# Kernel tuning notes

Hardware: AMD Instinct MI355X
Metric: run time of the kernel (lower is better)

## Reference

```python
import jax, jax.numpy as jnp
import numpy as np

HEADS = 8
DIM_HEAD = 64
SLICE = 64
DIM = 128
INNER = HEADS * DIM_HEAD
B, H, W = 4, 128, 128


def _conv(x_nchw, w_oihw, b):
    y = jax.lax.conv_general_dilated(
        x_nchw, w_oihw, window_strides=(1, 1), padding='SAME',
        dimension_numbers=('NCHW', 'OIHW', 'NCHW'))
    return y + b[None, :, None, None]


def setup_inputs() -> dict:
    key = jax.random.key(0)
    ks = jax.random.split(key, 10)
    s = lambda fan: 1.0 / np.sqrt(fan)
    return {
        'x': jax.random.normal(ks[0], (B, H, W, DIM), jnp.float32),
        'temperature': jnp.ones((1, HEADS, 1, 1), jnp.float32) * 0.5,
        'Wx': jax.random.normal(ks[1], (INNER, DIM, 3, 3), jnp.float32) * s(DIM * 9),
        'bx': jnp.zeros((INNER,), jnp.float32),
        'Wfx': jax.random.normal(ks[2], (INNER, DIM, 3, 3), jnp.float32) * s(DIM * 9),
        'bfx': jnp.zeros((INNER,), jnp.float32),
        'Ws': jax.random.normal(ks[3], (SLICE, DIM_HEAD), jnp.float32) * s(DIM_HEAD),
        'bs': jnp.zeros((SLICE,), jnp.float32),
        'Wq': jax.random.normal(ks[4], (DIM_HEAD, DIM_HEAD), jnp.float32) * s(DIM_HEAD),
        'Wk': jax.random.normal(ks[5], (DIM_HEAD, DIM_HEAD), jnp.float32) * s(DIM_HEAD),
        'Wv': jax.random.normal(ks[6], (DIM_HEAD, DIM_HEAD), jnp.float32) * s(DIM_HEAD),
        'Wo': jax.random.normal(ks[7], (DIM, INNER), jnp.float32) * s(INNER),
        'bo': jnp.zeros((DIM,), jnp.float32),
    }


def reference(x, temperature, Wx, bx, Wfx, bfx, Ws, bs, Wq, Wk, Wv, Wo, bo):
    b, h, w, _ = x.shape
    n = h * w
    scale = DIM_HEAD ** -0.5
    x_nchw = jnp.transpose(x, (0, 3, 1, 2))
    # conv projections -> [B, heads, N, dim_head]
    def to_heads(y):
        y = jnp.transpose(y, (0, 2, 3, 1)).reshape(b, n, HEADS, DIM_HEAD)
        return jnp.transpose(y, (0, 2, 1, 3))
    fx_mid = to_heads(_conv(x_nchw, Wfx, bfx))
    x_mid = to_heads(_conv(x_nchw, Wx, bx))
    # slice routing: softmax over M, temperature-scaled
    temp = jnp.clip(temperature, 0.1, 5.0)  # [1,heads,1,1]
    logits = (jnp.einsum('bhnc,gc->bhng', x_mid, Ws) + bs) / temp
    slice_weights = jax.nn.softmax(logits, axis=-1)  # [B,h,N,M]
    slice_norm = slice_weights.sum(axis=2)  # [B,h,M]
    slice_token = jnp.einsum('bhnc,bhng->bhgc', fx_mid, slice_weights)
    slice_token = slice_token / (slice_norm + 1e-5)[..., None]
    # small M x M attention over slice tokens
    q = jnp.einsum('bhgc,dc->bhgd', slice_token, Wq)
    k = jnp.einsum('bhgc,dc->bhgd', slice_token, Wk)
    v = jnp.einsum('bhgc,dc->bhgd', slice_token, Wv)
    dots = jnp.einsum('bhgd,bhkd->bhgk', q, k) * scale
    attn = jax.nn.softmax(dots, axis=-1)
    out_slice = jnp.einsum('bhgk,bhkd->bhgd', attn, v)
    # scatter back to points
    out_x = jnp.einsum('bhgc,bhng->bhnc', out_slice, slice_weights)
    out_x = jnp.transpose(out_x, (0, 2, 1, 3)).reshape(b, h, w, INNER)
    return jnp.einsum('bhwi,oi->bhwo', out_x, Wo) + bo
```

## Files before the change

### kernel.cpp

```cpp
#include <hip/hip_runtime.h>
#include <hip/hip_bf16.h>
#include <math.h>

#define B_ 4
#define H_ 128
#define W_ 128
#define DIM_ 128
#define HEADS_ 8
#define DH_ 64
#define G_ 64
#define INNER_ 512
#define N_ 16384

typedef __attribute__((ext_vector_type(8))) short sh8;
typedef __attribute__((ext_vector_type(4))) float vf4;

#define XPT_SLAB 4160
#define XPT_PLANE 2163200
#define WT_PLANE 1179648

__device__ __forceinline__ void gload16(const void* g, void* l) {
  __builtin_amdgcn_global_load_lds((const __attribute__((address_space(1))) void*)g,
                                   (__attribute__((address_space(3))) void*)l, 16, 0, 0);
}

__device__ __forceinline__ void split_bf16(float v, ushort& h, ushort& l) {
  __hip_bfloat16 hb = __float2bfloat16(v);
  float hf = __bfloat162float(hb);
  __hip_bfloat16 lb = __float2bfloat16(v - hf);
  h = *reinterpret_cast<ushort*>(&hb);
  l = *reinterpret_cast<ushort*>(&lb);
}

__global__ __launch_bounds__(256) void pad_tile_kernel(const float* __restrict__ x,
                                                       ushort* __restrict__ xpth,
                                                       ushort* __restrict__ xptl) {
  const int bz = blockIdx.y;
  x += (size_t)bz * N_ * DIM_;
  xpth += (size_t)bz * XPT_PLANE;
  xptl += (size_t)bz * XPT_PLANE;
  const int idx = blockIdx.x * 256 + threadIdx.x;
  const int row = idx / (4 * XPT_SLAB);
  const int rem = idx % (4 * XPT_SLAB);
  const int c0i = rem / XPT_SLAB;
  const int t2 = rem % XPT_SLAB;
  const int tile = t2 >> 3, j = t2 & 7;
  const int kg = tile / 130, px = tile % 130;
  const int c = c0i * 32 + kg * 8 + j;
  float v = 0.0f;
  if (row >= 1 && row <= H_ && px >= 1 && px <= W_)
    v = x[((size_t)(row - 1) * W_ + (px - 1)) * DIM_ + c];
  ushort hh, ll;
  split_bf16(v, hh, ll);
  xpth[idx] = hh;
  xptl[idx] = ll;
}

__global__ __launch_bounds__(256) void wfx_kernel(const float* __restrict__ Wfx,
                                                  ushort* __restrict__ wth,
                                                  ushort* __restrict__ wtl) {
  int idx = blockIdx.x * 256 + threadIdx.x;
  if (idx >= 9 * 512 * DIM_) return;
  const int c = idx & 127;
  const int ocf = (idx >> 7) & 511;
  const int tap = idx >> 16;
  float v = Wfx[((size_t)ocf * DIM_ + c) * 9 + tap];
  ushort hh, ll;
  split_bf16(v, hh, ll);
  const int nt = 4 + (ocf >> 7), oci = ocf & 127;
  const int c0i = c >> 5, kg = (c >> 3) & 3, j = c & 7;
  const size_t o = (((size_t)tap * 8 + nt) * 4 + c0i) * 4096 + ((size_t)kg * 128 + oci) * 8 + j;
  wth[o] = hh;
  wtl[o] = ll;
}

__global__ __launch_bounds__(256) void wcomp_kernel(const float* __restrict__ Wx,
                                                    const float* __restrict__ Ws,
                                                    const float* __restrict__ bx,
                                                    const float* __restrict__ bs,
                                                    const float* __restrict__ temperature,
                                                    ushort* __restrict__ wth,
                                                    ushort* __restrict__ wtl,
                                                    float* __restrict__ bc) {
  __shared__ float WxL[64][128];
  __shared__ float WsL[64][64];
  const int t = threadIdx.x;
  const int tap = blockIdx.x, h = blockIdx.y;
  for (int e = t; e < 8192; e += 256) {
    const int c2 = e >> 7, c = e & 127;
    WxL[c2][c] = Wx[((size_t)(h * 64 + c2) * DIM_ + c) * 9 + tap];
  }
  for (int e = t; e < 4096; e += 256) WsL[e >> 6][e & 63] = Ws[e];
  float tmp = fminf(fmaxf(temperature[h], 0.1f), 5.0f);
  const float invt = 1.0f / tmp;
  __syncthreads();
  for (int e = t; e < 8192; e += 256) {
    const int gg = e >> 7, c = e & 127;
    float s = 0.f;
#pragma unroll
    for (int c2 = 0; c2 < 64; ++c2) s = fmaf(WsL[gg][c2], WxL[c2][c], s);
    s *= invt;
    ushort hh, ll;
    split_bf16(s, hh, ll);
    const int ocp = h * 64 + gg;
    const int nt = ocp >> 7, oci = ocp & 127;
    const int c0i = c >> 5, kg = (c >> 3) & 3, j = c & 7;
    const size_t o = (((size_t)tap * 8 + nt) * 4 + c0i) * 4096 + ((size_t)kg * 128 + oci) * 8 + j;
    wth[o] = hh;
    wtl[o] = ll;
  }
  if (tap == 0 && t < 64) {
    float s = 0.f;
#pragma unroll
    for (int c2 = 0; c2 < 64; ++c2) s = fmaf(Ws[t * 64 + c2], bx[h * 64 + c2], s);
    bc[h * 64 + t] = (s + bs[t]) * invt;
  }
}

__global__ __launch_bounds__(256) void mqk_kernel(const float* __restrict__ Wq,
                                                  const float* __restrict__ Wk,
                                                  float* __restrict__ mqk) {
  const int idx = blockIdx.x * 256 + threadIdx.x;
  const int c = idx >> 6, c2 = idx & 63;
  float s = 0.f;
#pragma unroll
  for (int d = 0; d < 64; ++d) s = fmaf(Wq[d * 64 + c], Wk[d * 64 + c2], s);
  mqk[idx] = s * 0.125f;
}

__global__ __launch_bounds__(256) void conv_mfma_kernel(
    const ushort* __restrict__ xpth, const ushort* __restrict__ xptl,
    const ushort* __restrict__ wth, const ushort* __restrict__ wtl,
    const float* __restrict__ bc, const float* __restrict__ bfx,
    float* __restrict__ lg, float* __restrict__ fxo) {
  __shared__ __align__(16) ushort lds[16512];
  const int bz = blockIdx.z;
  xpth += (size_t)bz * XPT_PLANE;
  xptl += (size_t)bz * XPT_PLANE;
  lg += (size_t)bz * N_ * INNER_;
  fxo += (size_t)bz * N_ * INNER_;
  const int t = threadIdx.x;
  const int lane = t & 63;
  const int wid = t >> 6;
  const int wm = wid & 1, wn = wid >> 1;
  const int nt = blockIdx.x;
  const int y = blockIdx.y;
  const int col = lane & 15, quad = lane >> 4;

  vf4 acc[4][4];
#pragma unroll
  for (int i = 0; i < 4; ++i)
#pragma unroll
    for (int j = 0; j < 4; ++j) acc[i][j] = vf4{0.f, 0.f, 0.f, 0.f};

  auto stageB = [&](int tap, int c0i) {
    const size_t boff = (((size_t)tap * 8 + nt) * 4 + c0i) * 4096;
    gload16(wth + boff + t * 8, lds + 8320 + t * 8);
    gload16(wth + boff + 2048 + t * 8, lds + 8320 + 2048 + t * 8);
    gload16(wtl + boff + t * 8, lds + 12416 + t * 8);
    gload16(wtl + boff + 2048 + t * 8, lds + 12416 + 2048 + t * 8);
  };

  for (int ky = 0; ky < 3; ++ky) {
    for (int c0i = 0; c0i < 4; ++c0i) {
      const size_t aoff = ((size_t)(y + ky) * 4 + c0i) * XPT_SLAB;
      __syncthreads();
      gload16(xpth + aoff + t * 8, lds + t * 8);
      gload16(xpth + aoff + 2048 + t * 8, lds + 2048 + t * 8);
      gload16(xptl + aoff + t * 8, lds + 4160 + t * 8);
      gload16(xptl + aoff + 2048 + t * 8, lds + 4160 + 2048 + t * 8);
      if (t < 8) {
        *reinterpret_cast<sh8*>(lds + 4096 + t * 8) =
            *reinterpret_cast<const sh8*>(xpth + aoff + 4096 + t * 8);
        *reinterpret_cast<sh8*>(lds + 4160 + 4096 + t * 8) =
            *reinterpret_cast<const sh8*>(xptl + aoff + 4096 + t * 8);
      }
      stageB(ky * 3, c0i);
      __syncthreads();
      for (int kx = 0; kx < 3; ++kx) {
        sh8 ah[4], al[4], bh[4], bl[4];
#pragma unroll
        for (int j = 0; j < 4; ++j) {
          const int brd = (quad * 128 + wn * 64 + j * 16 + col) * 8;
          bh[j] = *reinterpret_cast<const sh8*>(lds + 8320 + brd);
          bl[j] = *reinterpret_cast<const sh8*>(lds + 12416 + brd);
        }
#pragma unroll
        for (int i = 0; i < 4; ++i) {
          const int ard = (quad * 130 + wm * 64 + i * 16 + col + kx) * 8;
          ah[i] = *reinterpret_cast<const sh8*>(lds + ard);
          al[i] = *reinterpret_cast<const sh8*>(lds + 4160 + ard);
        }
        if (kx < 2) {
          __syncthreads();
          stageB(ky * 3 + kx + 1, c0i);
        }
        __builtin_amdgcn_s_setprio(1);
#pragma unroll
        for (int i = 0; i < 4; ++i)
#pragma unroll
          for (int j = 0; j < 4; ++j) {
            acc[i][j] = __builtin_amdgcn_mfma_f32_16x16x32_bf16(ah[i], bh[j], acc[i][j], 0, 0, 0);
            acc[i][j] = __builtin_amdgcn_mfma_f32_16x16x32_bf16(ah[i], bl[j], acc[i][j], 0, 0, 0);
            acc[i][j] = __builtin_amdgcn_mfma_f32_16x16x32_bf16(al[i], bh[j], acc[i][j], 0, 0, 0);
          }
        __builtin_amdgcn_s_setprio(0);
        if (kx < 2) __syncthreads();
      }
    }
  }
  const bool first = (nt < 4);
  float* outp = first ? lg : fxo;
  const float* bb = first ? bc : bfx;
  const int ocbase = (nt & 3) * 128 + wn * 64 + col;
#pragma unroll
  for (int j = 0; j < 4; ++j) {
    const int oc = ocbase + j * 16;
    const float bv = bb[oc];
#pragma unroll
    for (int i = 0; i < 4; ++i) {
#pragma unroll
      for (int r = 0; r < 4; ++r) {
        const int px = wm * 64 + i * 16 + quad * 4 + r;
        outp[((size_t)(y * W_ + px)) * INNER_ + oc] = acc[i][j][r] + bv;
      }
    }
  }
}

__device__ __forceinline__ void fma16(float (&acc)[4][4], const float4 a, const float4 b) {
  acc[0][0] = fmaf(a.x, b.x, acc[0][0]);
  acc[0][1] = fmaf(a.x, b.y, acc[0][1]);
  acc[0][2] = fmaf(a.x, b.z, acc[0][2]);
  acc[0][3] = fmaf(a.x, b.w, acc[0][3]);
  acc[1][0] = fmaf(a.y, b.x, acc[1][0]);
  acc[1][1] = fmaf(a.y, b.y, acc[1][1]);
  acc[1][2] = fmaf(a.y, b.z, acc[1][2]);
  acc[1][3] = fmaf(a.y, b.w, acc[1][3]);
  acc[2][0] = fmaf(a.z, b.x, acc[2][0]);
  acc[2][1] = fmaf(a.z, b.y, acc[2][1]);
  acc[2][2] = fmaf(a.z, b.z, acc[2][2]);
  acc[2][3] = fmaf(a.z, b.w, acc[2][3]);
  acc[3][0] = fmaf(a.w, b.x, acc[3][0]);
  acc[3][1] = fmaf(a.w, b.y, acc[3][1]);
  acc[3][2] = fmaf(a.w, b.z, acc[3][2]);
  acc[3][3] = fmaf(a.w, b.w, acc[3][3]);
}

__global__ __launch_bounds__(256) void slice_kernel(float* __restrict__ lg,
                                                    const float* __restrict__ fxg,
                                                    float* __restrict__ tpart,
                                                    float* __restrict__ npart) {
  __shared__ __align__(16) float wl[64][68];
  __shared__ __align__(16) float fxl[64][68];
  __shared__ float red[8][64];
  const int bz = blockIdx.y;
  lg += (size_t)bz * N_ * INNER_;
  fxg += (size_t)bz * N_ * INNER_;
  tpart += (size_t)bz * 512 * 4096;
  npart += (size_t)bz * 512 * 64;
  unsigned int* lgp = reinterpret_cast<unsigned int*>(lg);

  const int t = threadIdx.x;
  const int sub = blockIdx.x & 63;
  const int h = blockIdx.x >> 6;
  const int nbase = sub * 256;
  const int tx = t & 15;
  const int ty = t >> 4;
  const int sn = t >> 2;
  const int sq = t & 3;
  const int gg2 = t & 63;
  const int q2 = t >> 6;

  float acc2[4][4] = {};
  float snrmp = 0.0f;

  for (int s = 0; s < 4; ++s) {
    const int n0 = nbase + s * 64;
    __syncthreads();
    {
      const int cg = t & 15;
      const int nr = t >> 4;
#pragma unroll
      for (int r = 0; r < 4; ++r) {
        const int nn = nr + r * 16;
        const size_t rowoff = ((size_t)(n0 + nn)) * INNER_ + h * DH_ + cg * 4;
        *reinterpret_cast<float4*>(&wl[nn][cg * 4]) =
            *reinterpret_cast<const float4*>(lg + rowoff);
        *reinterpret_cast<float4*>(&fxl[nn][cg * 4]) =
            *reinterpret_cast<const float4*>(fxg + rowoff);
      }
    }
    __syncthreads();
    float m = -3.4e38f;
#pragma unroll
    for (int jj = 0; jj < 16; ++jj) m = fmaxf(m, wl[sn][sq * 16 + jj]);
    red[sq][sn] = m;
    __syncthreads();
    m = fmaxf(fmaxf(red[0][sn], red[1][sn]), fmaxf(red[2][sn], red[3][sn]));
    float ss = 0.0f;
#pragma unroll
    for (int jj = 0; jj < 16; ++jj) {
      const float e = __expf(wl[sn][sq * 16 + jj] - m);
      wl[sn][sq * 16 + jj] = e;
      ss += e;
    }
    red[4 + sq][sn] = ss;
    __syncthreads();
    const float inv = 1.0f / (red[4][sn] + red[5][sn] + red[6][sn] + red[7][sn]);
#pragma unroll
    for (int jj = 0; jj < 16; ++jj) wl[sn][sq * 16 + jj] *= inv;
    __syncthreads();
    {
      const int gg = t & 15;
      const int nr = t >> 4;
#pragma unroll
      for (int r = 0; r < 4; ++r) {
        const int nn = nr + r * 16;
        uint4 pk;
        unsigned int* pp = reinterpret_cast<unsigned int*>(&pk);
#pragma unroll
        for (int j = 0; j < 4; ++j) {
          ushort hh, ll;
          split_bf16(wl[nn][gg * 4 + j], hh, ll);
          pp[j] = ((unsigned int)hh << 16) | (unsigned int)ll;
        }
        *reinterpret_cast<uint4*>(lgp + ((size_t)(n0 + nn)) * INNER_ + h * DH_ + gg * 4) = pk;
      }
    }
#pragma unroll
    for (int nn = 0; nn < 16; ++nn) snrmp += wl[q2 * 16 + nn][gg2];
#pragma unroll
    for (int kk = 0; kk < 64; ++kk) {
      const float4 a4 = *reinterpret_cast<const float4*>(&wl[kk][ty * 4]);
      const float4 b4 = *reinterpret_cast<const float4*>(&fxl[kk][tx * 4]);
      fma16(acc2, a4, b4);
    }
  }
  __syncthreads();
  red[q2][gg2] = snrmp;
  float* tp = tpart + (size_t)blockIdx.x * 4096;
#pragma unroll
  for (int i = 0; i < 4; ++i) {
    float4 v;
    v.x = acc2[i][0];
    v.y = acc2[i][1];
    v.z = acc2[i][2];
    v.w = acc2[i][3];
    *reinterpret_cast<float4*>(tp + (ty * 4 + i) * 64 + tx * 4) = v;
  }
  __syncthreads();
  if (t < 64)
    npart[(size_t)blockIdx.x * 64 + t] = red[0][t] + red[1][t] + red[2][t] + red[3][t];
}

__global__ __launch_bounds__(256) void reduce_kernel(const float* __restrict__ tpart,
                                                     const float* __restrict__ npart,
                                                     float* __restrict__ tok,
                                                     float* __restrict__ nrm) {
  const int bz = blockIdx.y;
  tpart += (size_t)bz * 512 * 4096;
  npart += (size_t)bz * 512 * 64;
  tok += (size_t)bz * (HEADS_ * G_ * DH_);
  nrm += (size_t)bz * (HEADS_ * G_);
  if (blockIdx.x < 128) {
    const int idx = blockIdx.x * 256 + threadIdx.x;
    const int h = idx >> 12, e = idx & 4095;
    float s = 0.f;
    for (int cb = 0; cb < 64; ++cb)
      s += tpart[(((size_t)(h * 64 + cb)) << 12) + e];
    tok[idx] = s;
  } else {
    for (int o = threadIdx.x; o < 512; o += 256) {
      const int h = o >> 6, g = o & 63;
      float s = 0.f;
      for (int cb = 0; cb < 64; ++cb) s += npart[(size_t)(h * 64 + cb) * 64 + g];
      nrm[o] = s;
    }
  }
}

__global__ __launch_bounds__(256) void head_kernel(const float* __restrict__ tok,
                                                   const float* __restrict__ nrm,
                                                   const float* __restrict__ mqk,
                                                   const float* __restrict__ Wv,
                                                   const float* __restrict__ Wo,
                                                   ushort* __restrict__ mht,
                                                   ushort* __restrict__ mlt) {
  __shared__ float ST[64 * 65];
  __shared__ float YL[64 * 64];
  __shared__ float VL[64 * 64];
  __shared__ float red[8][64];
  const int bz = blockIdx.y;
  tok += (size_t)bz * (HEADS_ * G_ * DH_);
  nrm += (size_t)bz * (HEADS_ * G_);
  mht += (size_t)bz * (INNER_ * DIM_);
  mlt += (size_t)bz * (INNER_ * DIM_);
  const int t = threadIdx.x;
  const int h = blockIdx.x;

  for (int e = t; e < 4096; e += 256) {
    const int g = e >> 6, c = e & 63;
    ST[g * 65 + c] = tok[(size_t)h * 4096 + e] / (nrm[h * 64 + g] + 1e-5f);
  }
  __syncthreads();
  for (int e = t; e < 4096; e += 256) {
    const int k = e >> 6, c = e & 63;
    float sy = 0.f, sv = 0.f;
    const float* mrow = mqk + c * 64;
    const float* wrow = Wv + c * 64;
#pragma unroll
    for (int c2 = 0; c2 < 64; ++c2) {
      const float st2 = ST[k * 65 + c2];
      sy = fmaf(mrow[c2], st2, sy);
      sv = fmaf(wrow[c2], st2, sv);
    }
    YL[k * 64 + c] = sy;
    VL[k * 64 + c] = sv;
  }
  __syncthreads();
  const int g = t & 63, kp = t >> 6;
  float z[16];
#pragma unroll
  for (int j = 0; j < 16; ++j) z[j] = 0.f;
  for (int c = 0; c < 64; ++c) {
    const float sg = ST[g * 65 + c];
#pragma unroll
    for (int j = 0; j < 16; ++j) z[j] = fmaf(sg, YL[(kp * 16 + j) * 64 + c], z[j]);
  }
  float m = z[0];
#pragma unroll
  for (int j = 1; j < 16; ++j) m = fmaxf(m, z[j]);
  red[kp][g] = m;
  __syncthreads();
  m = fmaxf(fmaxf(red[0][g], red[1][g]), fmaxf(red[2][g], red[3][g]));
  float ssum = 0.f;
#pragma unroll
  for (int j = 0; j < 16; ++j) {
    z[j] = __expf(z[j] - m);
    ssum += z[j];
  }
  red[4 + kp][g] = ssum;
  __syncthreads();
  ssum = red[4][g] + red[5][g] + red[6][g] + red[7][g];
  const float inv = 1.f / ssum;
#pragma unroll
  for (int j = 0; j < 16; ++j) ST[(kp * 16 + j) * 65 + g] = z[j] * inv;
  __syncthreads();
  for (int e = t; e < 4096; e += 256) {
    const int gg = e >> 6, d = e & 63;
    float s = 0.f;
#pragma unroll
    for (int k = 0; k < 64; ++k) s = fmaf(ST[k * 65 + gg], VL[k * 64 + d], s);
    YL[gg * 64 + d] = s;
  }
  __syncthreads();
  for (int e = t; e < 8192; e += 256) {
    const int o = e & 127, gg = e >> 7;
    float s = 0.f;
    const float* wrow = Wo + (size_t)o * INNER_ + h * 64;
#pragma unroll
    for (int d = 0; d < 64; ++d) s = fmaf(YL[gg * 64 + d], wrow[d], s);
    ushort hh, ll;
    split_bf16(s, hh, ll);
    const int hg = h * 64 + gg;
    const int kg2 = hg >> 3, kr = hg & 7;
    mht[((size_t)kg2 * 128 + o) * 8 + kr] = hh;
    mlt[((size_t)kg2 * 128 + o) * 8 + kr] = ll;
  }
}

__global__ __launch_bounds__(256) void fused_out_kernel(
    const unsigned int* __restrict__ wp,
    const ushort* __restrict__ mht,
    const ushort* __restrict__ mlt,
    const float* __restrict__ bo,
    float* __restrict__ out) {
  __shared__ __align__(16) ushort lds[24576];
  const int bz = blockIdx.y;
  wp += (size_t)bz * N_ * INNER_;
  mht += (size_t)bz * (INNER_ * DIM_);
  mlt += (size_t)bz * (INNER_ * DIM_);
  out += (size_t)bz * N_ * DIM_;
  const int t = threadIdx.x;
  const int lane = t & 63;
  const int wid = t >> 6;
  const int wm = wid & 1, wn = wid >> 1;
  const int col = lane & 15, quad = lane >> 4;
  const int n0 = blockIdx.x * 64;

  vf4 acc[2][4];
#pragma unroll
  for (int m = 0; m < 2; ++m)
#pragma unroll
    for (int n = 0; n < 4; ++n) acc[m][n] = vf4{0.f, 0.f, 0.f, 0.f};

  for (int kc = 0; kc < 8; ++kc) {
    __syncthreads();
#pragma unroll
    for (int r = 0; r < 2; ++r) {
      const int row = r * 256 + t;
      const int pix = row >> 3, kg2 = row & 7;
      const unsigned int* gp = wp + (size_t)(n0 + pix) * INNER_ + kc * 64 + kg2 * 8;
      const uint4 p0 = *reinterpret_cast<const uint4*>(gp);
      const uint4 p1 = *reinterpret_cast<const uint4*>(gp + 4);
      unsigned int u[8] = {p0.x, p0.y, p0.z, p0.w, p1.x, p1.y, p1.z, p1.w};
      sh8 hv, lv;
#pragma unroll
      for (int j = 0; j < 8; ++j) {
        hv[j] = (short)(u[j] >> 16);
        lv[j] = (short)(u[j] & 0xffff);
      }
      const int drow = pix * 8 + (kg2 ^ (pix & 7));
      *reinterpret_cast<sh8*>(lds + drow * 8) = hv;
      *reinterpret_cast<sh8*>(lds + 4096 + drow * 8) = lv;
    }
#pragma unroll
    for (int r = 0; r < 4; ++r) {
      gload16(mht + (size_t)kc * 8192 + ((size_t)r * 256 + t) * 8, lds + 8192 + r * 2048 + t * 8);
      gload16(mlt + (size_t)kc * 8192 + ((size_t)r * 256 + t) * 8, lds + 16384 + r * 2048 + t * 8);
    }
    __syncthreads();
#pragma unroll
    for (int kk = 0; kk < 2; ++kk) {
      const int kg2 = kk * 4 + quad;
      sh8 ah[2], al[2], bh[4], bl[4];
#pragma unroll
      for (int m = 0; m < 2; ++m) {
        const int pix = wm * 32 + m * 16 + col;
        const int drow = pix * 8 + (kg2 ^ (pix & 7));
        ah[m] = *reinterpret_cast<const sh8*>(lds + drow * 8);
        al[m] = *reinterpret_cast<const sh8*>(lds + 4096 + drow * 8);
      }
#pragma unroll
      for (int n = 0; n < 4; ++n) {
        const int o = wn * 64 + n * 16 + col;
        bh[n] = *reinterpret_cast<const sh8*>(lds + 8192 + ((size_t)kg2 * 128 + o) * 8);
        bl[n] = *reinterpret_cast<const sh8*>(lds + 16384 + ((size_t)kg2 * 128 + o) * 8);
      }
      __builtin_amdgcn_s_setprio(1);
#pragma unroll
      for (int m = 0; m < 2; ++m)
#pragma unroll
        for (int n = 0; n < 4; ++n) {
          acc[m][n] = __builtin_amdgcn_mfma_f32_16x16x32_bf16(ah[m], bh[n], acc[m][n], 0, 0, 0);
          acc[m][n] = __builtin_amdgcn_mfma_f32_16x16x32_bf16(ah[m], bl[n], acc[m][n], 0, 0, 0);
          acc[m][n] = __builtin_amdgcn_mfma_f32_16x16x32_bf16(al[m], bh[n], acc[m][n], 0, 0, 0);
        }
      __builtin_amdgcn_s_setprio(0);
    }
  }
#pragma unroll
  for (int n = 0; n < 4; ++n) {
    const int o = wn * 64 + n * 16 + col;
    const float bv = bo[o];
#pragma unroll
    for (int m = 0; m < 2; ++m) {
#pragma unroll
      for (int r = 0; r < 4; ++r) {
        const int pix = wm * 32 + m * 16 + quad * 4 + r;
        out[(size_t)(n0 + pix) * DIM_ + o] = acc[m][n][r] + bv;
      }
    }
  }
}

extern "C" void kernel_launch(void* const* d_in, const int* in_sizes, int n_in,
                              void* d_out, int out_size, void* d_ws, size_t ws_size,
                              hipStream_t stream) {
  const float* x    = (const float*)d_in[0];
  const float* temp = (const float*)d_in[1];
  const float* Wx   = (const float*)d_in[2];
  const float* bx   = (const float*)d_in[3];
  const float* Wfx  = (const float*)d_in[4];
  const float* bfx  = (const float*)d_in[5];
  const float* Ws   = (const float*)d_in[6];
  const float* bs   = (const float*)d_in[7];
  const float* Wq   = (const float*)d_in[8];
  const float* Wk   = (const float*)d_in[9];
  const float* Wv   = (const float*)d_in[10];
  const float* Wo   = (const float*)d_in[11];
  const float* bo   = (const float*)d_in[12];
  float* out = (float*)d_out;

  auto need = [](int nb) -> size_t {
    size_t s = 0;
    s += 2 * (size_t)WT_PLANE * 2;
    s += 2 * (size_t)nb * XPT_PLANE * 2;
    s += 2 * (size_t)nb * N_ * INNER_ * 4;
    s += (size_t)B_ * HEADS_ * G_ * DH_ * 4;
    s += (size_t)B_ * HEADS_ * G_ * 4;
    s += (size_t)DH_ * DH_ * 4;
    s += (size_t)INNER_ * 4;
    s += 2 * (size_t)nb * INNER_ * DIM_ * 2;
    s += (size_t)nb * 512 * 4096 * 4;
    s += (size_t)nb * 512 * 64 * 4;
    return s;
  };
  int nb = 1;
  if (ws_size >= need(4)) nb = 4;
  else if (ws_size >= need(2)) nb = 2;

  char* p = (char*)d_ws;
  ushort* WTH = (ushort*)p; p += (size_t)WT_PLANE * 2;
  ushort* WTL = (ushort*)p; p += (size_t)WT_PLANE * 2;
  ushort* XPTH = (ushort*)p; p += (size_t)nb * XPT_PLANE * 2;
  ushort* XPTL = (ushort*)p; p += (size_t)nb * XPT_PLANE * 2;
  float* LG  = (float*)p; p += (size_t)nb * N_ * INNER_ * 4;
  float* FXO = (float*)p; p += (size_t)nb * N_ * INNER_ * 4;
  float* TOK = (float*)p; p += (size_t)B_ * HEADS_ * G_ * DH_ * 4;
  float* NRM = (float*)p; p += (size_t)B_ * HEADS_ * G_ * 4;
  float* MQK = (float*)p; p += (size_t)DH_ * DH_ * 4;
  float* BC  = (float*)p; p += (size_t)INNER_ * 4;
  ushort* MHT = (ushort*)p; p += (size_t)nb * INNER_ * DIM_ * 2;
  ushort* MLT = (ushort*)p; p += (size_t)nb * INNER_ * DIM_ * 2;
  float* TP  = (float*)p; p += (size_t)nb * 512 * 4096 * 4;
  float* NP  = (float*)p; p += (size_t)nb * 512 * 64 * 4;

  wfx_kernel<<<2304, 256, 0, stream>>>(Wfx, WTH, WTL);
  wcomp_kernel<<<dim3(9, 8), 256, 0, stream>>>(Wx, Ws, bx, bs, temp, WTH, WTL, BC);
  mqk_kernel<<<16, 256, 0, stream>>>(Wq, Wk, MQK);

  for (int b0 = 0; b0 < B_; b0 += nb) {
    const float* xb = x + (size_t)b0 * N_ * DIM_;
    float* outb = out + (size_t)b0 * N_ * DIM_;
    float* tokb = TOK + (size_t)b0 * HEADS_ * G_ * DH_;
    float* nrmb = NRM + (size_t)b0 * HEADS_ * G_;

    pad_tile_kernel<<<dim3(8450, nb), 256, 0, stream>>>(xb, XPTH, XPTL);
    conv_mfma_kernel<<<dim3(8, 128, nb), 256, 0, stream>>>(XPTH, XPTL, WTH, WTL, BC, bfx, LG, FXO);
    slice_kernel<<<dim3(512, nb), 256, 0, stream>>>(LG, FXO, TP, NP);
    reduce_kernel<<<dim3(129, nb), 256, 0, stream>>>(TP, NP, tokb, nrmb);
    head_kernel<<<dim3(8, nb), 256, 0, stream>>>(tokb, nrmb, MQK, Wv, Wo, MHT, MLT);
    fused_out_kernel<<<dim3(256, nb), 256, 0, stream>>>((const unsigned int*)LG, MHT, MLT, bo, outb);
  }
}
```

Baseline: 763.3 us.

## Double-buffer input slab in conv MFMA kernel to overlap loads with compute

The conv kernel's activation slab moves into two LDS buffers. The next slab is prefetched during the kx=0 step of the current slab, and the first weight tile of the next slab is loaded during the last kx step. This removes the per-slab barrier-and-load stall that used to sit between the channel/row iterations, and the synchronous tail copy becomes an async global_load_lds. LDS use per block rises from about 33KB to about 50KB, which could lower occupancy.

```diff
diff --git a/kernel.cpp b/kernel.cpp
--- a/kernel.cpp
+++ b/kernel.cpp
@@ -133,7 +133,7 @@
     const ushort* __restrict__ wth, const ushort* __restrict__ wtl,
     const float* __restrict__ bc, const float* __restrict__ bfx,
     float* __restrict__ lg, float* __restrict__ fxo) {
-  __shared__ __align__(16) ushort lds[16512];
+  __shared__ __align__(16) ushort lds[24832];
   const int bz = blockIdx.z;
   xpth += (size_t)bz * XPT_PLANE;
   xptl += (size_t)bz * XPT_PLANE;
@@ -153,60 +153,66 @@
 #pragma unroll
     for (int j = 0; j < 4; ++j) acc[i][j] = vf4{0.f, 0.f, 0.f, 0.f};
 
-  auto stageB = [&](int tap, int c0i) {
+  auto stageA = [&](int p, int buf) {
+    const int ky = p >> 2, c0i = p & 3;
+    const size_t aoff = ((size_t)(y + ky) * 4 + c0i) * XPT_SLAB;
+    const int base = buf * 8320;
+    gload16(xpth + aoff + t * 8, lds + base + t * 8);
+    gload16(xpth + aoff + 2048 + t * 8, lds + base + 2048 + t * 8);
+    gload16(xptl + aoff + t * 8, lds + base + 4160 + t * 8);
+    gload16(xptl + aoff + 2048 + t * 8, lds + base + 4160 + 2048 + t * 8);
+    if (t < 8) {
+      gload16(xpth + aoff + 4096 + t * 8, lds + base + 4096 + t * 8);
+      gload16(xptl + aoff + 4096 + t * 8, lds + base + 4160 + 4096 + t * 8);
+    }
+  };
+  auto stageB = [&](int p, int kx) {
+    const int tap = (p >> 2) * 3 + kx;
+    const int c0i = p & 3;
     const size_t boff = (((size_t)tap * 8 + nt) * 4 + c0i) * 4096;
-    gload16(wth + boff + t * 8, lds + 8320 + t * 8);
-    gload16(wth + boff + 2048 + t * 8, lds + 8320 + 2048 + t * 8);
-    gload16(wtl + boff + t * 8, lds + 12416 + t * 8);
-    gload16(wtl + boff + 2048 + t * 8, lds + 12416 + 2048 + t * 8);
+    gload16(wth + boff + t * 8, lds + 16640 + t * 8);
+    gload16(wth + boff + 2048 + t * 8, lds + 16640 + 2048 + t * 8);
+    gload16(wtl + boff + t * 8, lds + 20736 + t * 8);
+    gload16(wtl + boff + 2048 + t * 8, lds + 20736 + 2048 + t * 8);
   };
 
-  for (int ky = 0; ky < 3; ++ky) {
-    for (int c0i = 0; c0i < 4; ++c0i) {
-      const size_t aoff = ((size_t)(y + ky) * 4 + c0i) * XPT_SLAB;
-      __syncthreads();
-      gload16(xpth + aoff + t * 8, lds + t * 8);
-      gload16(xpth + aoff + 2048 + t * 8, lds + 2048 + t * 8);
-      gload16(xptl + aoff + t * 8, lds + 4160 + t * 8);
-      gload16(xptl + aoff + 2048 + t * 8, lds + 4160 + 2048 + t * 8);
-      if (t < 8) {
-        *reinterpret_cast<sh8*>(lds + 4096 + t * 8) =
-            *reinterpret_cast<const sh8*>(xpth + aoff + 4096 + t * 8);
-        *reinterpret_cast<sh8*>(lds + 4160 + 4096 + t * 8) =
-            *reinterpret_cast<const sh8*>(xptl + aoff + 4096 + t * 8);
-      }
-      stageB(ky * 3, c0i);
-      __syncthreads();
-      for (int kx = 0; kx < 3; ++kx) {
-        sh8 ah[4], al[4], bh[4], bl[4];
+  stageA(0, 0);
+  stageB(0, 0);
+  __syncthreads();
+  for (int p = 0; p < 12; ++p) {
+    const int abase = (p & 1) * 8320;
+    for (int kx = 0; kx < 3; ++kx) {
+      sh8 ah[4], al[4], bh[4], bl[4];
+#pragma unroll
+      for (int j = 0; j < 4; ++j) {
+        const int brd = (quad * 128 + wn * 64 + j * 16 + col) * 8;
+        bh[j] = *reinterpret_cast<const sh8*>(lds + 16640 + brd);
+        bl[j] = *reinterpret_cast<const sh8*>(lds + 20736 + brd);
+      }
+#pragma unroll
+      for (int i = 0; i < 4; ++i) {
+        const int ard = (quad * 130 + wm * 64 + i * 16 + col + kx) * 8;
+        ah[i] = *reinterpret_cast<const sh8*>(lds + abase + ard);
+        al[i] = *reinterpret_cast<const sh8*>(lds + abase + 4160 + ard);
+      }
+      const bool more = (kx < 2) || (p < 11);
+      if (more) {
+        __syncthreads();
+        if (kx == 0 && p < 11) stageA(p + 1, (p + 1) & 1);
+        if (kx < 2) stageB(p, kx + 1);
+        else stageB(p + 1, 0);
+      }
+      __builtin_amdgcn_s_setprio(1);
+#pragma unroll
+      for (int i = 0; i < 4; ++i)
 #pragma unroll
         for (int j = 0; j < 4; ++j) {
-          const int brd = (quad * 128 + wn * 64 + j * 16 + col) * 8;
-          bh[j] = *reinterpret_cast<const sh8*>(lds + 8320 + brd);
-          bl[j] = *reinterpret_cast<const sh8*>(lds + 12416 + brd);
+          acc[i][j] = __builtin_amdgcn_mfma_f32_16x16x32_bf16(ah[i], bh[j], acc[i][j], 0, 0, 0);
+          acc[i][j] = __builtin_amdgcn_mfma_f32_16x16x32_bf16(ah[i], bl[j], acc[i][j], 0, 0, 0);
+          acc[i][j] = __builtin_amdgcn_mfma_f32_16x16x32_bf16(al[i], bh[j], acc[i][j], 0, 0, 0);
         }
-#pragma unroll
-        for (int i = 0; i < 4; ++i) {
-          const int ard = (quad * 130 + wm * 64 + i * 16 + col + kx) * 8;
-          ah[i] = *reinterpret_cast<const sh8*>(lds + ard);
-          al[i] = *reinterpret_cast<const sh8*>(lds + 4160 + ard);
-        }
-        if (kx < 2) {
-          __syncthreads();
-          stageB(ky * 3 + kx + 1, c0i);
-        }
-        __builtin_amdgcn_s_setprio(1);
-#pragma unroll
-        for (int i = 0; i < 4; ++i)
-#pragma unroll
-          for (int j = 0; j < 4; ++j) {
-            acc[i][j] = __builtin_amdgcn_mfma_f32_16x16x32_bf16(ah[i], bh[j], acc[i][j], 0, 0, 0);
-            acc[i][j] = __builtin_amdgcn_mfma_f32_16x16x32_bf16(ah[i], bl[j], acc[i][j], 0, 0, 0);
-            acc[i][j] = __builtin_amdgcn_mfma_f32_16x16x32_bf16(al[i], bh[j], acc[i][j], 0, 0, 0);
-          }
-        __builtin_amdgcn_s_setprio(0);
-        if (kx < 2) __syncthreads();
-      }
+      __builtin_amdgcn_s_setprio(0);
+      if (more) __syncthreads();
     }
   }
   const bool first = (nt < 4);
```

After: 749.4 us. About the same (-1.8%).
